# Kernel tuning notes

Hardware: AMD Instinct MI355X
Metric: run time of the kernel (lower is better)

The kernel has to match this reference:

```python
import jax, jax.numpy as jnp
import numpy as np
import math

D_MODEL = 1024
N_HEADS = 16
D_K = D_MODEL // N_HEADS
B, T = 4, 2048


def setup_inputs() -> dict:
    key = jax.random.key(0)
    ks = jax.random.split(key, 6)
    scale = 1.0 / math.sqrt(D_MODEL)
    x = jax.random.normal(ks[0], (B, T, D_MODEL), dtype=jnp.float32)
    Wq_w = jax.random.normal(ks[1], (D_MODEL, D_MODEL), dtype=jnp.float32) * scale
    Wk_w = jax.random.normal(ks[2], (D_MODEL, D_MODEL), dtype=jnp.float32) * scale
    Wv_w = jax.random.normal(ks[3], (D_MODEL, D_MODEL), dtype=jnp.float32) * scale
    Wo_w = jax.random.normal(ks[4], (D_MODEL, D_MODEL), dtype=jnp.float32) * scale
    zb = jnp.zeros((D_MODEL,), dtype=jnp.float32)
    # causal mask [1,1,T,T]: 1 where attention allowed (lower triangular)
    mask = jnp.tril(jnp.ones((T, T), dtype=jnp.int32))[None, None, :, :]
    return {
        "x": x, "mask": mask,
        "Wq_w": Wq_w, "Wq_b": zb, "Wk_w": Wk_w, "Wk_b": zb,
        "Wv_w": Wv_w, "Wv_b": zb, "Wo_w": Wo_w, "Wo_b": zb,
    }


def reference(x, mask, Wq_w, Wq_b, Wk_w, Wk_b, Wv_w, Wv_b, Wo_w, Wo_b):
    Bs, Ts, C = x.shape
    # nn.Linear: y = x @ W.T + b
    q = (x @ Wq_w.T + Wq_b).reshape(Bs, Ts, N_HEADS, D_K).transpose(0, 2, 1, 3)
    k = (x @ Wk_w.T + Wk_b).reshape(Bs, Ts, N_HEADS, D_K).transpose(0, 2, 1, 3)
    v = (x @ Wv_w.T + Wv_b).reshape(Bs, Ts, N_HEADS, D_K).transpose(0, 2, 1, 3)
    # scores: [B, H, T, T]
    scores = jnp.einsum('bhqd,bhkd->bhqk', q, k) / math.sqrt(D_K)
    scores = jnp.where(mask == 0, -jnp.inf, scores)
    probs = jax.nn.softmax(scores, axis=-1)
    # dropout=0 (eval) -> identity
    out = jnp.einsum('bhqk,bhkd->bhqd', probs, v)
    out = out.transpose(0, 2, 1, 3).reshape(Bs, Ts, C)
    return out @ Wo_w.T + Wo_b
```

## Files before the change

kernel.cpp:

```cpp
#include <hip/hip_runtime.h>


#define AS1 __attribute__((address_space(1)))
#define AS3 __attribute__((address_space(3)))

typedef __attribute__((ext_vector_type(8))) short bf16x8;
typedef __attribute__((ext_vector_type(4))) float f32x4;

constexpr int T_SEQ = 2048;
constexpr int DMODEL = 1024;
constexpr int NH = 16;
constexpr int DK = 64;

#if __has_builtin(__builtin_amdgcn_exp2f)
#define EXP2(x) __builtin_amdgcn_exp2f(x)
#else
#define EXP2(x) exp2f(x)
#endif
#if __has_builtin(__builtin_amdgcn_rcpf)
#define RCP(x) __builtin_amdgcn_rcpf(x)
#else
#define RCP(x) (1.0f / (x))
#endif

__device__ __forceinline__ unsigned short f2bf(float f) {
  union { float f; unsigned u; } v; v.f = f;
  return (unsigned short)((v.u + 0x7fffu + ((v.u >> 16) & 1u)) >> 16);
}

__global__ void cast_f32_bf16(const float4* __restrict__ in, ushort4* __restrict__ out, int n4) {
  int i = blockIdx.x * blockDim.x + threadIdx.x;
  if (i < n4) {
    float4 f = in[i];
    ushort4 o;
    o.x = f2bf(f.x); o.y = f2bf(f.y); o.z = f2bf(f.z); o.w = f2bf(f.w);
    out[i] = o;
  }
}

__global__ void cast_w4(const float4* __restrict__ a, const float4* __restrict__ b,
                        const float4* __restrict__ c, const float4* __restrict__ d,
                        ushort4* __restrict__ oa, ushort4* __restrict__ ob,
                        ushort4* __restrict__ oc, ushort4* __restrict__ od, int n4) {
  int i = blockIdx.x * blockDim.x + threadIdx.x;
  if (i >= n4) return;
  const float4* src = (blockIdx.y == 0) ? a : (blockIdx.y == 1) ? b : (blockIdx.y == 2) ? c : d;
  ushort4* dst = (blockIdx.y == 0) ? oa : (blockIdx.y == 1) ? ob : (blockIdx.y == 2) ? oc : od;
  float4 f = src[i];
  ushort4 o;
  o.x = f2bf(f.x); o.y = f2bf(f.y); o.z = f2bf(f.z); o.w = f2bf(f.w);
  dst[i] = o;
}

__device__ __forceinline__ void gload_lds16(const ushort* g, ushort* l) {
  __builtin_amdgcn_global_load_lds((AS1 void*)g, (AS3 void*)l, 16, 0, 0);
}

__device__ __forceinline__ void gemm_mainloop(
    const ushort* __restrict__ A, const ushort* __restrict__ Bw,
    ushort* As, ushort* Bs, int m0, int n0, f32x4 acc[4][4])
{
  const int t = threadIdx.x;
  const int lane = t & 63;
  const int wave = t >> 6;
  const int wm = (wave & 1) * 64;
  const int wn = (wave >> 1) * 64;
  const int lr = lane & 15;
  const int quad = lane >> 4;

  for (int k0 = 0; k0 < DMODEL; k0 += 32) {
    __syncthreads();
#pragma unroll
    for (int i = 0; i < 2; ++i) {
      const int c0 = i * 256 + wave * 64;
      const int c = c0 + lane;
      gload_lds16(A + (size_t)(m0 + (c >> 2)) * DMODEL + k0 + (c & 3) * 8, As + c0 * 8);
      gload_lds16(Bw + (size_t)(n0 + (c >> 2)) * DMODEL + k0 + (c & 3) * 8, Bs + c0 * 8);
    }
    __syncthreads();
    bf16x8 af[4], bfr[4];
#pragma unroll
    for (int mt = 0; mt < 4; ++mt)
      af[mt] = *(const bf16x8*)(As + (wm + mt * 16 + lr) * 32 + quad * 8);
#pragma unroll
    for (int nt = 0; nt < 4; ++nt)
      bfr[nt] = *(const bf16x8*)(Bs + (wn + nt * 16 + lr) * 32 + quad * 8);
#pragma unroll
    for (int mt = 0; mt < 4; ++mt)
#pragma unroll
      for (int nt = 0; nt < 4; ++nt)
        acc[mt][nt] = __builtin_amdgcn_mfma_f32_16x16x32_bf16(af[mt], bfr[nt], acc[mt][nt], 0, 0, 0);
  }
}

__global__ __launch_bounds__(256, 2) void gemm_qkv(
    const ushort* __restrict__ xb,
    const ushort* __restrict__ wq, const ushort* __restrict__ wk, const ushort* __restrict__ wv,
    const float* __restrict__ bq, const float* __restrict__ bk, const float* __restrict__ bv,
    ushort* __restrict__ Qb, ushort* __restrict__ Kb, ushort* __restrict__ Vt)
{
  __shared__ __align__(16) ushort As[128 * 32];
  __shared__ __align__(16) ushort Bs[128 * 32];
  const int n0 = blockIdx.x * 128;
  const int m0 = blockIdx.y * 128;
  const int z = blockIdx.z;
  const ushort* W = (z == 0) ? wq : (z == 1) ? wk : wv;
  const float* bias = (z == 0) ? bq : (z == 1) ? bk : bv;
  f32x4 acc[4][4] = {};
  gemm_mainloop(xb, W, As, Bs, m0, n0, acc);

  const int lane = threadIdx.x & 63;
  const int wave = threadIdx.x >> 6;
  const int wm = (wave & 1) * 64, wn = (wave >> 1) * 64;
  const int lr = lane & 15, quad = lane >> 4;
  const float scale = (z == 0) ? 0.1803368801111204f : 1.0f;
  ushort* dstQK = (z == 0) ? Qb : Kb;

#pragma unroll
  for (int mt = 0; mt < 4; ++mt) {
#pragma unroll
    for (int nt = 0; nt < 4; ++nt) {
      const int n = n0 + wn + nt * 16 + lr;
      const float bn = bias[n];
      const int h = n >> 6, d = n & 63;
      const int mb = m0 + wm + mt * 16 + quad * 4;
      const int b = mb >> 11, tt = mb & 2047;
      if (z < 2) {
#pragma unroll
        for (int r = 0; r < 4; ++r) {
          const float v = (acc[mt][nt][r] + bn) * scale;
          dstQK[((size_t)(b * NH + h) * T_SEQ + (tt + r)) * DK + d] = f2bf(v);
        }
      } else {
        ushort4 pk;
        pk.x = f2bf(acc[mt][nt][0] + bn);
        pk.y = f2bf(acc[mt][nt][1] + bn);
        pk.z = f2bf(acc[mt][nt][2] + bn);
        pk.w = f2bf(acc[mt][nt][3] + bn);
        *(ushort4*)&Vt[((size_t)(b * NH + h) * DK + d) * T_SEQ + tt] = pk;
      }
    }
  }
}

__global__ __launch_bounds__(128, 4) void attn_fwd(
    const ushort* __restrict__ Qb, const ushort* __restrict__ Kb,
    const ushort* __restrict__ Vt, ushort* __restrict__ attn)
{
  __shared__ __align__(16) ushort stage[2][2][2048];
  __shared__ float psd[2][16];
  const int u = blockIdx.x;
  const int bh = u & 63;
  const int qsub = 63 - (u >> 6);
  const int lane = threadIdx.x & 63;
  const int wv = threadIdx.x >> 6;
  const int lr = lane & 15, quad = lane >> 4;
  const int q0w = qsub * 32;
  const ushort* Qh = Qb + (size_t)bh * T_SEQ * DK;
  const ushort* Kh = Kb + (size_t)bh * T_SEQ * DK;
  const ushort* Vh = Vt + (size_t)bh * DK * T_SEQ;

  const int idx0 = (lr + ((lane & 16) ? 32 : 0)) << 2;
  const int idx1 = idx0 + 64;
  const bool hiHalf = (lane & 32) != 0;

  const int srow = lane >> 3;
  const int scol = ((lane & 7) ^ srow) * 8;
  const int c0 = (quad ^ (lr & 7)) * 8;
  const int c1 = c0 ^ 32;

  bf16x8 qf[2][2];
#pragma unroll
  for (int mf = 0; mf < 2; ++mf)
#pragma unroll
    for (int h = 0; h < 2; ++h)
      qf[mf][h] = *(const bf16x8*)(Qh + (size_t)(q0w + mf * 16 + lr) * DK + h * 32 + quad * 8);

  f32x4 o[2][4];
  float ps[2] = {0.f, 0.f};
#pragma unroll
  for (int mf = 0; mf < 2; ++mf)
#pragma unroll
    for (int nt = 0; nt < 4; ++nt) o[mf][nt] = (f32x4){0.f, 0.f, 0.f, 0.f};

  auto stageK = [&](int t, int buf) {
    const int kv0 = t * 32;
    ushort* dst = stage[wv][buf];
#pragma unroll
    for (int s = 0; s < 4; ++s)
      gload_lds16(Kh + (size_t)(kv0 + s * 8 + srow) * DK + scol, dst + s * 512);
  };

  auto compute = [&](int t, int buf) {
    const int kv0 = t * 32;
    const bool masked = (t == qsub);
    const ushort* kb = stage[wv][buf];
    bf16x8 vf[4];
#pragma unroll
    for (int nt = 0; nt < 4; ++nt)
      vf[nt] = *(const bf16x8*)(Vh + (size_t)(nt * 16 + lr) * T_SEQ + kv0 + quad * 8);

    unsigned pk[2][2][2];
#pragma unroll
    for (int cc = 0; cc < 2; ++cc) {
      const int kvc = kv0 + cc * 16;
      const bf16x8 kf0 = *(const bf16x8*)(kb + (cc * 16 + lr) * 64 + c0);
      const bf16x8 kf1 = *(const bf16x8*)(kb + (cc * 16 + lr) * 64 + c1);
#pragma unroll
      for (int mf = 0; mf < 2; ++mf) {
        f32x4 st = (f32x4){0.f, 0.f, 0.f, 0.f};
        st = __builtin_amdgcn_mfma_f32_16x16x32_bf16(kf0, qf[mf][0], st, 0, 0, 0);
        st = __builtin_amdgcn_mfma_f32_16x16x32_bf16(kf1, qf[mf][1], st, 0, 0, 0);
        float p[4];
#pragma unroll
        for (int r = 0; r < 4; ++r) {
          float e = EXP2(st[r]);
          if (masked) {
            const int ki = kvc + quad * 4 + r;
            const int qi = q0w + mf * 16 + lr;
            e = (ki <= qi) ? e : 0.f;
          }
          p[r] = e;
        }
        ps[mf] += (p[0] + p[1]) + (p[2] + p[3]);
        pk[mf][cc][0] = __builtin_amdgcn_perm(__float_as_uint(p[1]), __float_as_uint(p[0]), 0x07060302u);
        pk[mf][cc][1] = __builtin_amdgcn_perm(__float_as_uint(p[3]), __float_as_uint(p[2]), 0x07060302u);
      }
    }
#pragma unroll
    for (int mf = 0; mf < 2; ++mf) {
      int4 pr;
      {
        const int a = __builtin_amdgcn_ds_bpermute(idx0, (int)pk[mf][0][0]);
        const int b = __builtin_amdgcn_ds_bpermute(idx0, (int)pk[mf][1][0]);
        pr.x = hiHalf ? b : a;
      }
      {
        const int a = __builtin_amdgcn_ds_bpermute(idx0, (int)pk[mf][0][1]);
        const int b = __builtin_amdgcn_ds_bpermute(idx0, (int)pk[mf][1][1]);
        pr.y = hiHalf ? b : a;
      }
      {
        const int a = __builtin_amdgcn_ds_bpermute(idx1, (int)pk[mf][0][0]);
        const int b = __builtin_amdgcn_ds_bpermute(idx1, (int)pk[mf][1][0]);
        pr.z = hiHalf ? b : a;
      }
      {
        const int a = __builtin_amdgcn_ds_bpermute(idx1, (int)pk[mf][0][1]);
        const int b = __builtin_amdgcn_ds_bpermute(idx1, (int)pk[mf][1][1]);
        pr.w = hiHalf ? b : a;
      }
      union { int4 i; bf16x8 v; } pa;
      pa.i = pr;
#pragma unroll
      for (int nt = 0; nt < 4; ++nt)
        o[mf][nt] = __builtin_amdgcn_mfma_f32_16x16x32_bf16(pa.v, vf[nt], o[mf][nt], 0, 0, 0);
    }
  };

  {
    int ti = wv;
    if (ti <= qsub) {
      stageK(ti, 0);
      int buf = 0;
      while (true) {
        const int tn = ti + 2;
        asm volatile("s_waitcnt vmcnt(0)" ::: "memory");
        if (tn <= qsub) stageK(tn, buf ^ 1);
        compute(ti, buf);
        if (tn > qsub) break;
        ti = tn;
        buf ^= 1;
      }
    }
  }

#pragma unroll
  for (int mf = 0; mf < 2; ++mf) {
    float v = ps[mf];
    v += __shfl_xor(v, 16);
    v += __shfl_xor(v, 32);
    ps[mf] = v;
  }

  f32x4 okeep[4], odump[4];
  float pskeep, psdump;
  if (wv == 0) {
#pragma unroll
    for (int nt = 0; nt < 4; ++nt) { okeep[nt] = o[0][nt]; odump[nt] = o[1][nt]; }
    pskeep = ps[0]; psdump = ps[1];
  } else {
#pragma unroll
    for (int nt = 0; nt < 4; ++nt) { okeep[nt] = o[1][nt]; odump[nt] = o[0][nt]; }
    pskeep = ps[1]; psdump = ps[0];
  }

  float* dumpw = (float*)stage[wv];
#pragma unroll
  for (int nt = 0; nt < 4; ++nt)
#pragma unroll
    for (int r = 0; r < 4; ++r)
      dumpw[(quad * 4 + r) * 64 + nt * 16 + lr] = odump[nt][r];
  if (quad == 0) psd[wv][lr] = psdump;
  __syncthreads();

  const float* dumpo = (const float*)stage[1 - wv];
  const float tot = pskeep + psd[1 - wv][lr];
  const float inv = RCP(tot);
  float oo[4][4];
#pragma unroll
  for (int nt = 0; nt < 4; ++nt)
#pragma unroll
    for (int r = 0; r < 4; ++r)
      oo[nt][r] = okeep[nt][r] + dumpo[(quad * 4 + r) * 64 + nt * 16 + lr];
  __syncthreads();

  ushort* Po = (ushort*)stage;
#pragma unroll
  for (int r = 0; r < 4; ++r) {
    union { int i; float f; } iv;
    iv.i = __builtin_amdgcn_ds_bpermute((quad * 4 + r) << 2, __float_as_int(inv));
#pragma unroll
    for (int nt = 0; nt < 4; ++nt)
      Po[(wv * 16 + quad * 4 + r) * 64 + nt * 16 + lr] = f2bf(oo[nt][r] * iv.f);
  }

  const int b = bh >> 4, h = bh & 15;
#pragma unroll
  for (int it = 0; it < 2; ++it) {
    const int row = wv * 16 + it * 8 + (lane >> 3);
    const int col8 = (lane & 7) * 8;
    const int4 val = *(const int4*)(Po + row * 64 + col8);
    *(int4*)(attn + (size_t)(b * T_SEQ + q0w + row) * DMODEL + h * DK + col8) = val;
  }
}

__global__ __launch_bounds__(256, 2) void gemm_out(
    const ushort* __restrict__ attn, const ushort* __restrict__ wo,
    const float* __restrict__ bo, float* __restrict__ out)
{
  __shared__ __align__(16) ushort As[128 * 32];
  __shared__ __align__(16) ushort Bs[128 * 32];
  const int n0 = blockIdx.x * 128;
  const int m0 = blockIdx.y * 128;
  f32x4 acc[4][4] = {};
  gemm_mainloop(attn, wo, As, Bs, m0, n0, acc);
  const int lane = threadIdx.x & 63, wave = threadIdx.x >> 6;
  const int wm = (wave & 1) * 64, wn = (wave >> 1) * 64;
  const int lr = lane & 15, quad = lane >> 4;
#pragma unroll
  for (int mt = 0; mt < 4; ++mt)
#pragma unroll
    for (int nt = 0; nt < 4; ++nt) {
      const int n = n0 + wn + nt * 16 + lr;
      const float bn = bo[n];
#pragma unroll
      for (int r = 0; r < 4; ++r) {
        const int m = m0 + wm + mt * 16 + quad * 4 + r;
        out[(size_t)m * DMODEL + n] = acc[mt][nt][r] + bn;
      }
    }
}

extern "C" void kernel_launch(void* const* d_in, const int* in_sizes, int n_in,
                              void* d_out, int out_size, void* d_ws, size_t ws_size,
                              hipStream_t stream) {
  const float* x  = (const float*)d_in[0];
  const float* Wq = (const float*)d_in[2];
  const float* bq = (const float*)d_in[3];
  const float* Wk = (const float*)d_in[4];
  const float* bk = (const float*)d_in[5];
  const float* Wv = (const float*)d_in[6];
  const float* bv = (const float*)d_in[7];
  const float* Wo = (const float*)d_in[8];
  const float* bo = (const float*)d_in[9];
  float* out = (float*)d_out;

  const size_t MD = (size_t)8192 * 1024;
  const size_t WD = (size_t)1024 * 1024;
  ushort* ws  = (ushort*)d_ws;
  ushort* xb  = ws;
  ushort* wqb = xb + MD;
  ushort* wkb = wqb + WD;
  ushort* wvb = wkb + WD;
  ushort* wob = wvb + WD;
  ushort* Qb  = wob + WD;
  ushort* Kb  = Qb + MD;
  ushort* Vt  = Kb + MD;
  ushort* att = Vt + MD;

  cast_f32_bf16<<<8192, 256, 0, stream>>>((const float4*)x, (ushort4*)xb, (int)(MD / 4));
  cast_w4<<<dim3(1024, 4), 256, 0, stream>>>(
      (const float4*)Wq, (const float4*)Wk, (const float4*)Wv, (const float4*)Wo,
      (ushort4*)wqb, (ushort4*)wkb, (ushort4*)wvb, (ushort4*)wob, (int)(WD / 4));

  gemm_qkv<<<dim3(8, 64, 3), 256, 0, stream>>>(xb, wqb, wkb, wvb, bq, bk, bv, Qb, Kb, Vt);
  attn_fwd<<<4096, 128, 0, stream>>>(Qb, Kb, Vt, att);
  gemm_out<<<dim3(8, 64), 256, 0, stream>>>(att, wob, bo, out);
}
```

Measured before the change: 301.8 us.

## Stage QKV epilogue through LDS for coalesced stores; single-buffer K in attention

The QKV GEMM epilogue now writes bias-added bf16 tiles into a per-wave LDS buffer, then emits 16-byte coalesced global stores for Q/K rows and for the transposed V layout, replacing the scattered 2-byte and 8-byte stores. The attention kernel drops K double-buffering to a single per-wave LDS buffer, pads the reduction scratch to avoid bank conflicts, and raises launch bounds to 8 blocks per CU to gain occupancy. The trade-off is that K loads no longer overlap compute within a wave, so latency hiding depends on more resident waves, and the GEMM uses extra LDS which may lower its occupancy.

```diff
diff --git a/kernel.cpp b/kernel.cpp
--- a/kernel.cpp
+++ b/kernel.cpp
@@ -101,6 +101,7 @@
 {
   __shared__ __align__(16) ushort As[128 * 32];
   __shared__ __align__(16) ushort Bs[128 * 32];
+  __shared__ __align__(16) ushort ep[4][2560];
   const int n0 = blockIdx.x * 128;
   const int m0 = blockIdx.y * 128;
   const int z = blockIdx.z;
@@ -115,39 +116,71 @@
   const int lr = lane & 15, quad = lane >> 4;
   const float scale = (z == 0) ? 0.1803368801111204f : 1.0f;
   ushort* dstQK = (z == 0) ? Qb : Kb;
-
-#pragma unroll
-  for (int mt = 0; mt < 4; ++mt) {
-#pragma unroll
-    for (int nt = 0; nt < 4; ++nt) {
-      const int n = n0 + wn + nt * 16 + lr;
-      const float bn = bias[n];
-      const int h = n >> 6, d = n & 63;
-      const int mb = m0 + wm + mt * 16 + quad * 4;
-      const int b = mb >> 11, tt = mb & 2047;
-      if (z < 2) {
-#pragma unroll
-        for (int r = 0; r < 4; ++r) {
-          const float v = (acc[mt][nt][r] + bn) * scale;
-          dstQK[((size_t)(b * NH + h) * T_SEQ + (tt + r)) * DK + d] = f2bf(v);
+  ushort* myep = ep[wave];
+  const int hgrp = (n0 + wn) >> 6;
+  const int mbase = m0 + wm;
+  const int bidx = mbase >> 11;
+
+  float bn4[4];
+#pragma unroll
+  for (int nt = 0; nt < 4; ++nt) bn4[nt] = bias[n0 + wn + nt * 16 + lr];
+
+#pragma unroll
+  for (int ph = 0; ph < 2; ++ph) {
+    if (z < 2) {
+#pragma unroll
+      for (int mi = 0; mi < 2; ++mi) {
+        const int mt = ph * 2 + mi;
+#pragma unroll
+        for (int nt = 0; nt < 4; ++nt)
+#pragma unroll
+          for (int r = 0; r < 4; ++r)
+            myep[(mi * 16 + quad * 4 + r) * 72 + nt * 16 + lr] =
+                f2bf((acc[mt][nt][r] + bn4[nt]) * scale);
+      }
+      asm volatile("s_waitcnt lgkmcnt(0)" ::: "memory");
+#pragma unroll
+      for (int p = 0; p < 4; ++p) {
+        const int ml = p * 8 + (lane >> 3);
+        const int ck = (lane & 7) * 8;
+        const int4 v = *(const int4*)(myep + ml * 72 + ck);
+        const int tt = (mbase + ph * 32 + ml) & 2047;
+        *(int4*)(dstQK + (((size_t)(bidx * NH + hgrp) * T_SEQ + tt) << 6) + ck) = v;
+      }
+      asm volatile("s_waitcnt lgkmcnt(0)" ::: "memory");
+    } else {
+#pragma unroll
+      for (int mi = 0; mi < 2; ++mi) {
+        const int mt = ph * 2 + mi;
+#pragma unroll
+        for (int nt = 0; nt < 4; ++nt) {
+          ushort4 qv;
+          qv.x = f2bf(acc[mt][nt][0] + bn4[nt]);
+          qv.y = f2bf(acc[mt][nt][1] + bn4[nt]);
+          qv.z = f2bf(acc[mt][nt][2] + bn4[nt]);
+          qv.w = f2bf(acc[mt][nt][3] + bn4[nt]);
+          *(ushort4*)(myep + (nt * 16 + lr) * 40 + mi * 16 + quad * 4) = qv;
         }
-      } else {
-        ushort4 pk;
-        pk.x = f2bf(acc[mt][nt][0] + bn);
-        pk.y = f2bf(acc[mt][nt][1] + bn);
-        pk.z = f2bf(acc[mt][nt][2] + bn);
-        pk.w = f2bf(acc[mt][nt][3] + bn);
-        *(ushort4*)&Vt[((size_t)(b * NH + h) * DK + d) * T_SEQ + tt] = pk;
-      }
-    }
-  }
-}
-
-__global__ __launch_bounds__(128, 4) void attn_fwd(
+      }
+      asm volatile("s_waitcnt lgkmcnt(0)" ::: "memory");
+#pragma unroll
+      for (int p = 0; p < 4; ++p) {
+        const int nl = p * 16 + (lane >> 2);
+        const int ck = (lane & 3) * 8;
+        const int4 v = *(const int4*)(myep + nl * 40 + ck);
+        const int tb = (mbase + ph * 32) & 2047;
+        *(int4*)(Vt + (((size_t)(bidx * NH + hgrp) * DK + nl) << 11) + tb + ck) = v;
+      }
+      asm volatile("s_waitcnt lgkmcnt(0)" ::: "memory");
+    }
+  }
+}
+
+__global__ __launch_bounds__(128, 8) void attn_fwd(
     const ushort* __restrict__ Qb, const ushort* __restrict__ Kb,
     const ushort* __restrict__ Vt, ushort* __restrict__ attn)
 {
-  __shared__ __align__(16) ushort stage[2][2][2048];
+  __shared__ __align__(16) float smf[2][1056];
   __shared__ float psd[2][16];
   const int u = blockIdx.x;
   const int bh = u & 63;
@@ -159,6 +192,7 @@
   const ushort* Qh = Qb + (size_t)bh * T_SEQ * DK;
   const ushort* Kh = Kb + (size_t)bh * T_SEQ * DK;
   const ushort* Vh = Vt + (size_t)bh * DK * T_SEQ;
+  ushort* kbuf = (ushort*)smf[wv];
 
   const int idx0 = (lr + ((lane & 16) ? 32 : 0)) << 2;
   const int idx1 = idx0 + 64;
@@ -183,18 +217,16 @@
 #pragma unroll
     for (int nt = 0; nt < 4; ++nt) o[mf][nt] = (f32x4){0.f, 0.f, 0.f, 0.f};
 
-  auto stageK = [&](int t, int buf) {
+  auto stageK = [&](int t) {
     const int kv0 = t * 32;
-    ushort* dst = stage[wv][buf];
 #pragma unroll
     for (int s = 0; s < 4; ++s)
-      gload_lds16(Kh + (size_t)(kv0 + s * 8 + srow) * DK + scol, dst + s * 512);
+      gload_lds16(Kh + (size_t)(kv0 + s * 8 + srow) * DK + scol, kbuf + s * 512);
   };
 
-  auto compute = [&](int t, int buf) {
+  auto compute = [&](int t) {
     const int kv0 = t * 32;
     const bool masked = (t == qsub);
-    const ushort* kb = stage[wv][buf];
     bf16x8 vf[4];
 #pragma unroll
     for (int nt = 0; nt < 4; ++nt)
@@ -204,8 +236,8 @@
 #pragma unroll
     for (int cc = 0; cc < 2; ++cc) {
       const int kvc = kv0 + cc * 16;
-      const bf16x8 kf0 = *(const bf16x8*)(kb + (cc * 16 + lr) * 64 + c0);
-      const bf16x8 kf1 = *(const bf16x8*)(kb + (cc * 16 + lr) * 64 + c1);
+      const bf16x8 kf0 = *(const bf16x8*)(kbuf + (cc * 16 + lr) * 64 + c0);
+      const bf16x8 kf1 = *(const bf16x8*)(kbuf + (cc * 16 + lr) * 64 + c1);
 #pragma unroll
       for (int mf = 0; mf < 2; ++mf) {
         f32x4 st = (f32x4){0.f, 0.f, 0.f, 0.f};
@@ -261,16 +293,15 @@
   {
     int ti = wv;
     if (ti <= qsub) {
-      stageK(ti, 0);
-      int buf = 0;
+      stageK(ti);
       while (true) {
+        asm volatile("s_waitcnt vmcnt(0)" ::: "memory");
+        compute(ti);
         const int tn = ti + 2;
-        asm volatile("s_waitcnt vmcnt(0)" ::: "memory");
-        if (tn <= qsub) stageK(tn, buf ^ 1);
-        compute(ti, buf);
         if (tn > qsub) break;
+        asm volatile("s_waitcnt lgkmcnt(0)" ::: "memory");
+        stageK(tn);
         ti = tn;
-        buf ^= 1;
       }
     }
   }
@@ -295,16 +326,16 @@
     pskeep = ps[1]; psdump = ps[0];
   }
 
-  float* dumpw = (float*)stage[wv];
+  float* dumpw = smf[wv];
 #pragma unroll
   for (int nt = 0; nt < 4; ++nt)
 #pragma unroll
     for (int r = 0; r < 4; ++r)
-      dumpw[(quad * 4 + r) * 64 + nt * 16 + lr] = odump[nt][r];
+      dumpw[(quad * 4 + r) * 66 + nt * 16 + lr] = odump[nt][r];
   if (quad == 0) psd[wv][lr] = psdump;
   __syncthreads();
 
-  const float* dumpo = (const float*)stage[1 - wv];
+  const float* dumpo = smf[1 - wv];
   const float tot = pskeep + psd[1 - wv][lr];
   const float inv = RCP(tot);
   float oo[4][4];
@@ -312,10 +343,10 @@
   for (int nt = 0; nt < 4; ++nt)
 #pragma unroll
     for (int r = 0; r < 4; ++r)
-      oo[nt][r] = okeep[nt][r] + dumpo[(quad * 4 + r) * 64 + nt * 16 + lr];
+      oo[nt][r] = okeep[nt][r] + dumpo[(quad * 4 + r) * 66 + nt * 16 + lr];
   __syncthreads();
 
-  ushort* Po = (ushort*)stage;
+  ushort* Po = (ushort*)smf;
 #pragma unroll
   for (int r = 0; r < 4; ++r) {
     union { int i; float f; } iv;
```

After: 660.2 us. 119% more time.
